# Kernel tuning notes

Hardware: AMD Instinct MI355X
Metric: run time of the kernel (lower is better)

The kernel has to match this reference:

```python
import jax, jax.numpy as jnp
import numpy as np

N_NODES = 4096
N_HEADS = 8
NEG_SLOPE = 0.2  # PyG GATConv default leaky_relu slope


def _gat_single(h, src, dst, att_src, att_dst):
    # h: [N, H, C] projected node features; src/dst: [E] (self-loops included)
    a_s = (h * att_src).sum(-1)                      # [N, H]
    a_d = (h * att_dst).sum(-1)                      # [N, H]
    e = jax.nn.leaky_relu(a_s[src] + a_d[dst], NEG_SLOPE)   # [E, H]
    m = jax.ops.segment_max(e, dst, num_segments=N_NODES)   # [N, H]
    ex = jnp.exp(e - m[dst])                         # [E, H]
    denom = jax.ops.segment_sum(ex, dst, num_segments=N_NODES)
    alpha = ex / denom[dst]                          # [E, H] (self-loops => denom > 0)
    out = jax.ops.segment_sum(alpha[:, :, None] * h[src], dst, num_segments=N_NODES)
    return out                                       # [N, H, C]


def setup_inputs() -> dict:
    key = jax.random.key(0)
    ks = jax.random.split(key, 12)
    B, T, N, F = 4, 12, N_NODES, 8
    Hg, Hl = 64, 128
    inp = {
        "x": jax.random.normal(ks[0], (B, T, N, F), jnp.float32),
        "edge_index": jax.random.randint(ks[1], (2, 65536), 0, N, jnp.int64),
        "W_gat": jax.random.normal(ks[2], (F, Hg), jnp.float32) * 0.3,
        "att_src": jax.random.normal(ks[3], (N_HEADS, Hg // N_HEADS), jnp.float32) * 0.3,
        "att_dst": jax.random.normal(ks[4], (N_HEADS, Hg // N_HEADS), jnp.float32) * 0.3,
        "b_gat": jax.random.normal(ks[5], (Hg,), jnp.float32) * 0.1,
        "W_ih": jax.random.normal(ks[6], (4 * Hl, Hg * N), jnp.float32) * 0.002,
        "W_hh": jax.random.normal(ks[7], (4 * Hl, Hl), jnp.float32) * 0.05,
        "b_ih": jax.random.normal(ks[8], (4 * Hl,), jnp.float32) * 0.05,
        "b_hh": jax.random.normal(ks[9], (4 * Hl,), jnp.float32) * 0.05,
        "W_fc": jax.random.normal(ks[10], (Hl, N * F), jnp.float32) * 0.05,
        "b_fc": jax.random.normal(ks[11], (N * F,), jnp.float32) * 0.05,
    }
    return inp


def reference(x, edge_index, W_gat, att_src, att_dst, b_gat,
              W_ih, W_hh, b_ih, b_hh, W_fc, b_fc):
    B, T, N, F = x.shape
    H = N_HEADS
    C = W_gat.shape[1] // H
    Hl = W_hh.shape[1]

    # add self-loops (PyG GATConv default add_self_loops=True)
    loop = jnp.arange(N, dtype=edge_index.dtype)
    src = jnp.concatenate([edge_index[0], loop])
    dst = jnp.concatenate([edge_index[1], loop])

    # ---- GAT over all (batch, time) graphs at once ----
    h = (x.reshape(B * T, N, F) @ W_gat).reshape(B * T, N, H, C)
    gat = jax.vmap(_gat_single, in_axes=(0, None, None, None, None))(
        h, src, dst, att_src, att_dst)                # [BT, N, H, C]
    gat = gat.reshape(B * T, N, H * C) + b_gat
    gat = jax.nn.elu(gat)                             # dropout p=0 (eval) => identity
    seq = gat.reshape(B, T, N * H * C)

    # ---- LSTM (torch gate order: i, f, g, o) ----
    def step(carry, x_t):
        hprev, cprev = carry
        gates = x_t @ W_ih.T + b_ih + hprev @ W_hh.T + b_hh   # [B, 4Hl]
        i, f, g, o = jnp.split(gates, 4, axis=-1)
        c = jax.nn.sigmoid(f) * cprev + jax.nn.sigmoid(i) * jnp.tanh(g)
        hn = jax.nn.sigmoid(o) * jnp.tanh(c)
        return (hn, c), None

    h0 = jnp.zeros((B, Hl), x.dtype)
    (h_last, _), _ = jax.lax.scan(step, (h0, h0), seq.transpose(1, 0, 2))

    out = h_last @ W_fc + b_fc
    return out.reshape(B, N, F)
```

## Files before the change

kernel.cpp:

```cpp
#include <hip/hip_runtime.h>

#define NN 4096
#define NH 8
#define BTT 48
#define KG 262144
#define NJ 512
#define HLL 128
#define ERAW 65536
#define NKC 256
#define NG  24576

typedef __attribute__((ext_vector_type(8))) short bf16x8;
typedef __attribute__((ext_vector_type(4))) float f32x4;
typedef __attribute__((ext_vector_type(8))) unsigned short ushort8;

__device__ __forceinline__ unsigned short f2bf(float f) {
  unsigned int u = __float_as_uint(f);
  u += 0x7FFFu + ((u >> 16) & 1u);
  return (unsigned short)(u >> 16);
}
__device__ __forceinline__ float bf2f(unsigned short s) {
  return __uint_as_float(((unsigned int)s) << 16);
}
__device__ __forceinline__ float4 nt_load4(const float* p) {
  f32x4 v = __builtin_nontemporal_load((const f32x4*)p);
  return float4{v[0], v[1], v[2], v[3]};
}

__global__ __launch_bounds__(256) void k_sp(const float* __restrict__ x, const float* __restrict__ Wg,
                                            const float* __restrict__ att_s, const float* __restrict__ att_d,
                                            const int* __restrict__ ei, int* __restrict__ cursor,
                                            int* __restrict__ ssrc, float* __restrict__ G,
                                            unsigned short* __restrict__ h, float* __restrict__ a_s,
                                            float* __restrict__ a_d) {
  int tid = threadIdx.x;
  int bid = blockIdx.x;
  if (bid >= 6144) {
    int t = (bid - 6144) * 256 + tid;
    if (t < NG) G[t] = 0.f;
    if (t < ERAW) {
      int s = ei[t], d = ei[ERAW + t];
      int pos = atomicAdd(&cursor[d], 1);
      ssrc[(d << 6) + pos] = s;
    } else {
      int n = t - ERAW;
      int pos = atomicAdd(&cursor[n], 1);
      ssrc[(n << 6) + pos] = n;
    }
    return;
  }
  __shared__ float wgs[512];
  __shared__ float ats[64], atd[64];
  wgs[tid] = Wg[tid];
  wgs[256 + tid] = Wg[256 + tid];
  if (tid < 64) { ats[tid] = att_s[tid]; atd[tid] = att_d[tid]; }
  __syncthreads();
  int bt = bid >> 7;
  int inner = bid & 127;
  int hd = tid & 7, nl = tid >> 3;
  int n = inner * 32 + nl;
  const float* xr = x + ((size_t)(bt * NN + n)) * 8;
  float4 xa = *(const float4*)xr, xb2 = *(const float4*)(xr + 4);
  float xv[8] = {xa.x, xa.y, xa.z, xa.w, xb2.x, xb2.y, xb2.z, xb2.w};
  int hb = hd * 8;
  float hv[8];
#pragma unroll
  for (int c = 0; c < 8; ++c) {
    float acc = 0.f;
#pragma unroll
    for (int f = 0; f < 8; ++f) acc += xv[f] * wgs[f * 64 + hb + c];
    hv[c] = acc;
  }
  float as = 0.f, ad = 0.f;
#pragma unroll
  for (int c = 0; c < 8; ++c) { as += hv[c] * ats[hb + c]; ad += hv[c] * atd[hb + c]; }
  int aoff = bt * (NN * NH) + n * NH + hd;
  a_s[aoff] = as;
  a_d[aoff] = ad;
  ushort8 hr;
#pragma unroll
  for (int c = 0; c < 8; ++c) hr[c] = f2bf(hv[c]);
  *(ushort8*)(h + (size_t)bt * KG + (size_t)n * 64 + hb) = hr;
}

__global__ __launch_bounds__(256) void k_gat(const unsigned short* __restrict__ h, const float* __restrict__ a_s,
                                             const float* __restrict__ a_d, const int* __restrict__ cursor,
                                             const int* __restrict__ ssrc, const float* __restrict__ b_gat,
                                             unsigned short* __restrict__ Xb) {
  int B = blockIdx.x;
  int xcd = B & 7;
  int slot = B >> 3;
  int btg = slot >> 7;
  int inner = slot & 127;
  int bt = btg * 8 + xcd;
  int tid = threadIdx.x;
  int hd = tid & 7, nl = tid >> 3;
  int n = inner * 32 + nl;
  const unsigned short* hbase = h + (size_t)bt * KG;
  const float* asb = a_s + bt * (NN * NH);
  float adn = a_d[bt * (NN * NH) + n * NH + hd];
  int deg = cursor[n];
  const int* bucket = ssrc + (n << 6);
  float ssum = 0.f;
  float o[8];
#pragma unroll
  for (int c = 0; c < 8; ++c) o[c] = 0.f;
  for (int i = 0; i < deg; ++i) {
    int s = bucket[i];
    float e = asb[s * NH + hd] + adn;
    e = (e > 0.f) ? e : 0.2f * e;
    float p = __expf(e);
    ssum += p;
    ushort8 hvv = *(const ushort8*)(hbase + (size_t)s * 64 + hd * 8);
#pragma unroll
    for (int c = 0; c < 8; ++c) o[c] += p * bf2f(hvv[c]);
  }
  float inv = 1.f / ssum;
  ushort8 r;
#pragma unroll
  for (int c = 0; c < 8; ++c) {
    float v = o[c] * inv + b_gat[hd * 8 + c];
    v = (v > 0.f) ? v : (__expf(v) - 1.f);
    r[c] = f2bf(v);
  }
  *(ushort8*)(Xb + (size_t)bt * KG + (size_t)n * 64 + hd * 8) = r;
}

__global__ __launch_bounds__(256) void k_gemm(const unsigned short* __restrict__ Xb,
                                              const float* __restrict__ Wih, float* __restrict__ G) {
  int tid = threadIdx.x;
  int w = tid >> 6, lane = tid & 63;
  int lm = lane & 15, kg = lane >> 4;
  int jb = blockIdx.x & 3;
  int kc = blockIdx.x >> 2;
  int j0 = jb * 128 + w * 32;
  size_t kbase = (size_t)kc * 1024 + kg * 8;

  const float* wr0 = Wih + (size_t)(j0 + lm) * KG + kbase;
  const float* wr1 = Wih + (size_t)(j0 + 16 + lm) * KG + kbase;
  const short* Xs = (const short*)Xb;
  const short* xr0 = Xs + (size_t)lm * KG + kbase;
  const short* xr1 = xr0 + (size_t)16 * KG;
  const short* xr2 = xr0 + (size_t)32 * KG;

  f32x4 acc[3][2];
#pragma unroll
  for (int mf = 0; mf < 3; ++mf)
#pragma unroll
    for (int jf = 0; jf < 2; ++jf) acc[mf][jf] = f32x4{0.f, 0.f, 0.f, 0.f};

  float4 wbuf[2][4];
  bf16x8 abuf[2][3];

  wbuf[0][0] = nt_load4(wr0);
  wbuf[0][1] = nt_load4(wr0 + 4);
  wbuf[0][2] = nt_load4(wr1);
  wbuf[0][3] = nt_load4(wr1 + 4);
  abuf[0][0] = *(const bf16x8*)(xr0);
  abuf[0][1] = *(const bf16x8*)(xr1);
  abuf[0][2] = *(const bf16x8*)(xr2);

#pragma unroll 2
  for (int t = 0; t < 32; ++t) {
    int cur = t & 1, nxt = cur ^ 1;
    if (t + 1 < 32) {
      int off = (t + 1) * 32;
      wbuf[nxt][0] = nt_load4(wr0 + off);
      wbuf[nxt][1] = nt_load4(wr0 + off + 4);
      wbuf[nxt][2] = nt_load4(wr1 + off);
      wbuf[nxt][3] = nt_load4(wr1 + off + 4);
      abuf[nxt][0] = *(const bf16x8*)(xr0 + off);
      abuf[nxt][1] = *(const bf16x8*)(xr1 + off);
      abuf[nxt][2] = *(const bf16x8*)(xr2 + off);
    }
#pragma unroll
    for (int jf = 0; jf < 2; ++jf) {
      float4 f0 = wbuf[cur][jf * 2], f1 = wbuf[cur][jf * 2 + 1];
      bf16x8 bb;
      bb[0] = (short)f2bf(f0.x); bb[1] = (short)f2bf(f0.y);
      bb[2] = (short)f2bf(f0.z); bb[3] = (short)f2bf(f0.w);
      bb[4] = (short)f2bf(f1.x); bb[5] = (short)f2bf(f1.y);
      bb[6] = (short)f2bf(f1.z); bb[7] = (short)f2bf(f1.w);
      acc[0][jf] = __builtin_amdgcn_mfma_f32_16x16x32_bf16(abuf[cur][0], bb, acc[0][jf], 0, 0, 0);
      acc[1][jf] = __builtin_amdgcn_mfma_f32_16x16x32_bf16(abuf[cur][1], bb, acc[1][jf], 0, 0, 0);
      acc[2][jf] = __builtin_amdgcn_mfma_f32_16x16x32_bf16(abuf[cur][2], bb, acc[2][jf], 0, 0, 0);
    }
  }

#pragma unroll
  for (int mf = 0; mf < 3; ++mf)
#pragma unroll
    for (int jf = 0; jf < 2; ++jf) {
      int j = j0 + jf * 16 + lm;
#pragma unroll
      for (int r = 0; r < 4; ++r) {
        int bt = mf * 16 + kg * 4 + r;
        atomicAdd(&G[bt * NJ + j], acc[mf][jf][r]);
      }
    }
}

__global__ __launch_bounds__(512) void k_lstm(const float* __restrict__ G, const float* __restrict__ Whh,
                                              const float* __restrict__ bih, const float* __restrict__ bhh,
                                              float* __restrict__ hlast) {
  __shared__ float hs[HLL];
  __shared__ float gs[NJ];
  int b = blockIdx.x, j = threadIdx.x;
  float bias = bih[j] + bhh[j];
  float w[HLL];
  const float* wr = Whh + (size_t)j * HLL;
#pragma unroll
  for (int k = 0; k < HLL; k += 4) {
    float4 v = *(const float4*)(wr + k);
    w[k] = v.x; w[k + 1] = v.y; w[k + 2] = v.z; w[k + 3] = v.w;
  }
  if (j < HLL) hs[j] = 0.f;
  float c = 0.f;
  __syncthreads();
  for (int t = 0; t < 12; ++t) {
    float acc = G[(size_t)(b * 12 + t) * NJ + j] + bias;
#pragma unroll
    for (int k = 0; k < HLL; ++k) acc += w[k] * hs[k];
    gs[j] = acc;
    __syncthreads();
    if (j < HLL) {
      float gi = gs[j], gf = gs[HLL + j], gg = gs[2 * HLL + j], go = gs[3 * HLL + j];
      float si = 1.f / (1.f + __expf(-gi));
      float sf = 1.f / (1.f + __expf(-gf));
      float so = 1.f / (1.f + __expf(-go));
      c = sf * c + si * tanhf(gg);
      hs[j] = so * tanhf(c);
    }
    __syncthreads();
  }
  if (j < HLL) hlast[b * HLL + j] = hs[j];
}

__global__ __launch_bounds__(256) void k_fc(const float* __restrict__ hlast, const float* __restrict__ Wfc,
                                            const float* __restrict__ bfc, float* __restrict__ out) {
  __shared__ float hl[NJ];
  int tid = threadIdx.x;
  hl[tid] = hlast[tid];
  hl[256 + tid] = hlast[256 + tid];
  __syncthreads();
  int n = blockIdx.x * 256 + tid;
  float a0 = 0.f, a1 = 0.f, a2 = 0.f, a3 = 0.f;
#pragma unroll 8
  for (int k = 0; k < HLL; ++k) {
    float wv = Wfc[(size_t)k * 32768 + n];
    a0 += hl[k] * wv;
    a1 += hl[HLL + k] * wv;
    a2 += hl[2 * HLL + k] * wv;
    a3 += hl[3 * HLL + k] * wv;
  }
  float bb = bfc[n];
  out[n] = a0 + bb;
  out[32768 + n] = a1 + bb;
  out[65536 + n] = a2 + bb;
  out[98304 + n] = a3 + bb;
}

extern "C" void kernel_launch(void* const* d_in, const int* in_sizes, int n_in,
                              void* d_out, int out_size, void* d_ws, size_t ws_size,
                              hipStream_t stream) {
  const float* x     = (const float*)d_in[0];
  const int*   ei    = (const int*)d_in[1];
  const float* Wg    = (const float*)d_in[2];
  const float* att_s = (const float*)d_in[3];
  const float* att_d = (const float*)d_in[4];
  const float* b_gat = (const float*)d_in[5];
  const float* Wih   = (const float*)d_in[6];
  const float* Whh   = (const float*)d_in[7];
  const float* bih   = (const float*)d_in[8];
  const float* bhh   = (const float*)d_in[9];
  const float* Wfc   = (const float*)d_in[10];
  const float* bfc   = (const float*)d_in[11];
  float* out = (float*)d_out;

  char* ws = (char*)d_ws;
  unsigned short* h  = (unsigned short*)(ws);
  float* a_s         = (float*)(ws + 25165824);
  float* a_d         = (float*)(ws + 31457280);
  unsigned short* Xb = (unsigned short*)(ws + 37748736);
  int* ssrc          = (int*)(ws + 62914560);
  float* G           = (float*)(ws + 63963136);
  float* hlast       = (float*)(ws + 64061440);
  int* cursor        = (int*)(ws + 64063488);

  hipMemsetAsync(cursor, 0, NN * sizeof(int), stream);
  hipLaunchKernelGGL(k_sp,   dim3(6416),     dim3(256), 0, stream, x, Wg, att_s, att_d, ei, cursor, ssrc, G, h, a_s, a_d);
  hipLaunchKernelGGL(k_gat,  dim3(48 * 128), dim3(256), 0, stream, h, a_s, a_d, cursor, ssrc, b_gat, Xb);
  hipLaunchKernelGGL(k_gemm, dim3(1024),     dim3(256), 0, stream, Xb, Wih, G);
  hipLaunchKernelGGL(k_lstm, dim3(4),        dim3(512), 0, stream, G, Whh, bih, bhh, hlast);
  hipLaunchKernelGGL(k_fc,   dim3(128),      dim3(256), 0, stream, hlast, Wfc, bfc, out);
}
```

Measured before the change: 286.0 us.

## Split GEMM atomics into 8 partial buffers and fuse LSTM with FC

The GEMM's atomic accumulation into G is spread across 8 partial buffers, one per group of 32 k-chunks, to reduce atomic contention. The buffers are zeroed by the cursor memset instead of inside k_sp. The LSTM and FC kernels are merged into one 64-block kernel: every block redundantly runs the full 4-batch LSTM, summing the 8 partials, then computes its slice of the FC output. This removes one launch and the hlast round trip, but makes each block run the serial recurrence four times (4x12 steps instead of 12).

After: 410.3 us. 43.4% more time.

```diff
diff --git a/kernel.cpp b/kernel.cpp
--- a/kernel.cpp
+++ b/kernel.cpp
@@ -30,14 +30,13 @@
 __global__ __launch_bounds__(256) void k_sp(const float* __restrict__ x, const float* __restrict__ Wg,
                                             const float* __restrict__ att_s, const float* __restrict__ att_d,
                                             const int* __restrict__ ei, int* __restrict__ cursor,
-                                            int* __restrict__ ssrc, float* __restrict__ G,
+                                            int* __restrict__ ssrc,
                                             unsigned short* __restrict__ h, float* __restrict__ a_s,
                                             float* __restrict__ a_d) {
   int tid = threadIdx.x;
   int bid = blockIdx.x;
   if (bid >= 6144) {
     int t = (bid - 6144) * 256 + tid;
-    if (t < NG) G[t] = 0.f;
     if (t < ERAW) {
       int s = ei[t], d = ei[ERAW + t];
       int pos = atomicAdd(&cursor[d], 1);
@@ -127,7 +126,7 @@
 }
 
 __global__ __launch_bounds__(256) void k_gemm(const unsigned short* __restrict__ Xb,
-                                              const float* __restrict__ Wih, float* __restrict__ G) {
+                                              const float* __restrict__ Wih, float* __restrict__ Gp8) {
   int tid = threadIdx.x;
   int w = tid >> 6, lane = tid & 63;
   int lm = lane & 15, kg = lane >> 4;
@@ -187,6 +186,7 @@
     }
   }
 
+  float* gout = Gp8 + (size_t)(kc >> 5) * NG;
 #pragma unroll
   for (int mf = 0; mf < 3; ++mf)
 #pragma unroll
@@ -195,17 +195,19 @@
 #pragma unroll
       for (int r = 0; r < 4; ++r) {
         int bt = mf * 16 + kg * 4 + r;
-        atomicAdd(&G[bt * NJ + j], acc[mf][jf][r]);
+        atomicAdd(&gout[bt * NJ + j], acc[mf][jf][r]);
       }
     }
 }
 
-__global__ __launch_bounds__(512) void k_lstm(const float* __restrict__ G, const float* __restrict__ Whh,
+__global__ __launch_bounds__(512) void k_tail(const float* __restrict__ Gp8, const float* __restrict__ Whh,
                                               const float* __restrict__ bih, const float* __restrict__ bhh,
-                                              float* __restrict__ hlast) {
+                                              const float* __restrict__ Wfc, const float* __restrict__ bfc,
+                                              float* __restrict__ out) {
   __shared__ float hs[HLL];
   __shared__ float gs[NJ];
-  int b = blockIdx.x, j = threadIdx.x;
+  __shared__ float hl[4 * HLL];
+  int j = threadIdx.x;
   float bias = bih[j] + bhh[j];
   float w[HLL];
   const float* wr = Whh + (size_t)j * HLL;
@@ -214,36 +216,33 @@
     float4 v = *(const float4*)(wr + k);
     w[k] = v.x; w[k + 1] = v.y; w[k + 2] = v.z; w[k + 3] = v.w;
   }
-  if (j < HLL) hs[j] = 0.f;
-  float c = 0.f;
-  __syncthreads();
-  for (int t = 0; t < 12; ++t) {
-    float acc = G[(size_t)(b * 12 + t) * NJ + j] + bias;
-#pragma unroll
-    for (int k = 0; k < HLL; ++k) acc += w[k] * hs[k];
-    gs[j] = acc;
+  for (int b = 0; b < 4; ++b) {
+    if (j < HLL) hs[j] = 0.f;
+    float c = 0.f;
     __syncthreads();
-    if (j < HLL) {
-      float gi = gs[j], gf = gs[HLL + j], gg = gs[2 * HLL + j], go = gs[3 * HLL + j];
-      float si = 1.f / (1.f + __expf(-gi));
-      float sf = 1.f / (1.f + __expf(-gf));
-      float so = 1.f / (1.f + __expf(-go));
-      c = sf * c + si * tanhf(gg);
-      hs[j] = so * tanhf(c);
-    }
+    for (int t = 0; t < 12; ++t) {
+      const float* gp = Gp8 + (size_t)(b * 12 + t) * NJ + j;
+      float acc = bias;
+#pragma unroll
+      for (int s = 0; s < 8; ++s) acc += gp[(size_t)s * NG];
+#pragma unroll
+      for (int k = 0; k < HLL; ++k) acc += w[k] * hs[k];
+      gs[j] = acc;
+      __syncthreads();
+      if (j < HLL) {
+        float gi = gs[j], gf = gs[HLL + j], gg = gs[2 * HLL + j], go = gs[3 * HLL + j];
+        float si = 1.f / (1.f + __expf(-gi));
+        float sf = 1.f / (1.f + __expf(-gf));
+        float so = 1.f / (1.f + __expf(-go));
+        c = sf * c + si * tanhf(gg);
+        hs[j] = so * tanhf(c);
+      }
+      __syncthreads();
+    }
+    if (j < HLL) hl[b * HLL + j] = hs[j];
     __syncthreads();
   }
-  if (j < HLL) hlast[b * HLL + j] = hs[j];
-}
-
-__global__ __launch_bounds__(256) void k_fc(const float* __restrict__ hlast, const float* __restrict__ Wfc,
-                                            const float* __restrict__ bfc, float* __restrict__ out) {
-  __shared__ float hl[NJ];
-  int tid = threadIdx.x;
-  hl[tid] = hlast[tid];
-  hl[256 + tid] = hlast[256 + tid];
-  __syncthreads();
-  int n = blockIdx.x * 256 + tid;
+  int n = blockIdx.x * 512 + j;
   float a0 = 0.f, a1 = 0.f, a2 = 0.f, a3 = 0.f;
 #pragma unroll 8
   for (int k = 0; k < HLL; ++k) {
@@ -283,14 +282,12 @@
   float* a_d         = (float*)(ws + 31457280);
   unsigned short* Xb = (unsigned short*)(ws + 37748736);
   int* ssrc          = (int*)(ws + 62914560);
-  float* G           = (float*)(ws + 63963136);
-  float* hlast       = (float*)(ws + 64061440);
-  int* cursor        = (int*)(ws + 64063488);
-
-  hipMemsetAsync(cursor, 0, NN * sizeof(int), stream);
-  hipLaunchKernelGGL(k_sp,   dim3(6416),     dim3(256), 0, stream, x, Wg, att_s, att_d, ei, cursor, ssrc, G, h, a_s, a_d);
+  int* cursor        = (int*)(ws + 63963136);
+  float* Gp8         = (float*)(ws + 63979520);
+
+  hipMemsetAsync(cursor, 0, 16384 + 786432, stream);
+  hipLaunchKernelGGL(k_sp,   dim3(6416),     dim3(256), 0, stream, x, Wg, att_s, att_d, ei, cursor, ssrc, h, a_s, a_d);
   hipLaunchKernelGGL(k_gat,  dim3(48 * 128), dim3(256), 0, stream, h, a_s, a_d, cursor, ssrc, b_gat, Xb);
-  hipLaunchKernelGGL(k_gemm, dim3(1024),     dim3(256), 0, stream, Xb, Wih, G);
-  hipLaunchKernelGGL(k_lstm, dim3(4),        dim3(512), 0, stream, G, Whh, bih, bhh, hlast);
-  hipLaunchKernelGGL(k_fc,   dim3(128),      dim3(256), 0, stream, hlast, Wfc, bfc, out);
-}
+  hipLaunchKernelGGL(k_gemm, dim3(1024),     dim3(256), 0, stream, Xb, Wih, Gp8);
+  hipLaunchKernelGGL(k_tail, dim3(64),       dim3(512), 0, stream, Gp8, Whh, bih, bhh, Wfc, bfc, out);
+}
```
